# Kernel optimization log

Hardware: AMD Instinct MI355X
Metric: run time of the kernel (lower is better)

## Reference

```python
import jax, jax.numpy as jnp
import numpy as np

N_CLASS = 4432          # 1108 siRNA classes x 4 cell types
N_GROUPS = 4
GROUP_SIZE = N_CLASS // N_GROUPS  # 1108
LABEL_SMOOTHING = 0.1
CONFIDENCE = 1.0 - LABEL_SMOOTHING
SMOOTHING_VALUE = LABEL_SMOOTHING / (GROUP_SIZE - 1)


def setup_inputs() -> dict:
    key = jax.random.key(0)
    k1, k2 = jax.random.split(key)
    output = jax.random.normal(k1, (16384, N_CLASS), dtype=jnp.float32)
    target = jax.random.randint(k2, (16384,), 0, N_CLASS, dtype=jnp.int64)
    return {"output": output, "target": target}


def reference(output, target):
    # output: [B, C] logits, target: [B] int labels
    log_output = jax.nn.log_softmax(output, axis=1)                      # [B, C]
    classes = jnp.arange(N_CLASS, dtype=target.dtype)                    # [C]
    one_hot = jnp.where(classes[None, :] == target[:, None],
                        CONFIDENCE, SMOOTHING_VALUE).astype(output.dtype)  # [B, C]
    # group of each class (4 cell-type groups, contiguous blocks of GROUP_SIZE)
    class_group = classes // GROUP_SIZE                                  # [C]
    target_group = target // GROUP_SIZE                                  # [B]
    # zero smoothed mass for classes outside the sample's group (masks[group])
    one_hot = jnp.where(class_group[None, :] == target_group[:, None], one_hot, 0.0)
    loss = -(one_hot * log_output).sum(axis=1)                           # [B]
    return jnp.mean(loss)
```

## Files before the change

kernel.cpp:

```cpp
#include <hip/hip_runtime.h>
#include <math.h>

#define N_CLASS   4432
#define GROUP_SZ  1108
#define NV4       (N_CLASS / 4)
#define GV4       (GROUP_SZ / 4)
#define NROWS     16384
#define BLOCK     256
#define FULL_IT   17
#define TAIL_BASE (FULL_IT * 64)
#define TAIL_N    (NV4 - TAIL_BASE)

static constexpr float CONF   = 0.9f;
static constexpr float SMOOTH = 0.1f / (GROUP_SZ - 1);

typedef float v4f __attribute__((ext_vector_type(4)));

template <bool WS_MODE>
__global__ __launch_bounds__(BLOCK)
void lsl_kernel(const float* __restrict__ logits,
                const int*   __restrict__ target,
                float*       __restrict__ sink) {
    const int wave = threadIdx.x >> 6;
    const int lane = threadIdx.x & 63;
    const int row  = (NROWS - 1) - (blockIdx.x * 4 + wave);
    const v4f* __restrict__ rp = (const v4f*)(logits + (size_t)row * N_CLASS);

    const int t      = target[row];
    const int g      = t / GROUP_SZ;
    const int glo    = g * GV4;
    const int ghi    = glo + GV4;
    const int tchunk = t >> 2;
    const int tlane  = t & 3;

    v4f v[FULL_IT + 1];
    #pragma unroll
    for (int i = 0; i < FULL_IT; ++i)
        v[i] = __builtin_nontemporal_load(&rp[lane + 64 * i]);
    const bool have18 = (lane < TAIL_N);
    v[FULL_IT] = (v4f){-INFINITY, -INFINITY, -INFINITY, -INFINITY};
    if (have18) v[FULL_IT] = __builtin_nontemporal_load(&rp[TAIL_BASE + lane]);

    float m = -INFINITY;
    #pragma unroll
    for (int i = 0; i <= FULL_IT; ++i)
        m = fmaxf(m, fmaxf(fmaxf(v[i].x, v[i].y), fmaxf(v[i].z, v[i].w)));
    #pragma unroll
    for (int off = 32; off > 0; off >>= 1)
        m = fmaxf(m, __shfl_xor(m, off));

    float s = 0.f;
    #pragma unroll
    for (int i = 0; i <= FULL_IT; ++i) {
        s += __expf(v[i].x - m) + __expf(v[i].y - m)
           + __expf(v[i].z - m) + __expf(v[i].w - m);
    }

    float gsum = 0.f, xt = 0.f;
    #pragma unroll
    for (int i = 0; i <= FULL_IT; ++i) {
        const int  c     = (i < FULL_IT) ? (lane + 64 * i) : (TAIL_BASE + lane);
        const bool valid = (i < FULL_IT) || have18;
        if (valid && c >= glo && c < ghi)
            gsum += (v[i].x + v[i].y) + (v[i].z + v[i].w);
        if (valid && c == tchunk)
            xt = (tlane == 0) ? v[i].x : (tlane == 1) ? v[i].y
               : (tlane == 2) ? v[i].z : v[i].w;
    }

    #pragma unroll
    for (int off = 32; off > 0; off >>= 1) {
        s    += __shfl_xor(s, off);
        gsum += __shfl_xor(gsum, off);
        xt   += __shfl_xor(xt, off);
    }

    if (lane == 0) {
        const float loss = (m + __logf(s)) - ((CONF - SMOOTH) * xt + SMOOTH * gsum);
        if (WS_MODE) sink[row] = loss;
        else         atomicAdd(sink, loss * (1.0f / NROWS));
    }
}

__global__ __launch_bounds__(256)
void lsl_reduce(const float* __restrict__ ws, float* __restrict__ out) {
    const float4* wp = (const float4*)ws;
    const int tid = threadIdx.x;
    float s = 0.f;
    #pragma unroll
    for (int i = 0; i < NROWS / 4 / 256; ++i) {
        float4 v = wp[tid + i * 256];
        s += (v.x + v.y) + (v.z + v.w);
    }
    #pragma unroll
    for (int off = 32; off > 0; off >>= 1) s += __shfl_xor(s, off);
    __shared__ float ss[4];
    const int wave = tid >> 6, lane = tid & 63;
    if (lane == 0) ss[wave] = s;
    __syncthreads();
    if (tid == 0) out[0] = ((ss[0] + ss[1]) + (ss[2] + ss[3])) * (1.0f / NROWS);
}

extern "C" void kernel_launch(void* const* d_in, const int* in_sizes, int n_in,
                              void* d_out, int out_size, void* d_ws, size_t ws_size,
                              hipStream_t stream) {
    const float* logits = (const float*)d_in[0];
    const int*   target = (const int*)d_in[1];
    float*       result = (float*)d_out;
    float*       ws     = (float*)d_ws;

    if (ws_size >= (size_t)NROWS * sizeof(float)) {
        lsl_kernel<true><<<NROWS / 4, BLOCK, 0, stream>>>(logits, target, ws);
        lsl_reduce<<<1, 256, 0, stream>>>(ws, result);
    } else {
        hipMemsetAsync(result, 0, sizeof(float), stream);
        lsl_kernel<false><<<NROWS / 4, BLOCK, 0, stream>>>(logits, target, result);
    }
}
```

Measured before the change: 356.0 us.

## Map one row per 256-thread block with shared-memory cross-wave reduction

Measured after the change: 382.1 us. 1.07x slower.

```diff
diff --git a/kernel.cpp b/kernel.cpp
--- a/kernel.cpp
+++ b/kernel.cpp
@@ -7,9 +7,8 @@
 #define GV4       (GROUP_SZ / 4)
 #define NROWS     16384
 #define BLOCK     256
-#define FULL_IT   17
-#define TAIL_BASE (FULL_IT * 64)
-#define TAIL_N    (NV4 - TAIL_BASE)
+#define CPT       4
+#define TAIL_T    (NV4 - CPT * BLOCK)
 
 static constexpr float CONF   = 0.9f;
 static constexpr float SMOOTH = 0.1f / (GROUP_SZ - 1);
@@ -17,14 +16,20 @@
 typedef float v4f __attribute__((ext_vector_type(4)));
 
 template <bool WS_MODE>
-__global__ __launch_bounds__(BLOCK)
+__global__ __launch_bounds__(BLOCK, 8)
 void lsl_kernel(const float* __restrict__ logits,
                 const int*   __restrict__ target,
                 float*       __restrict__ sink) {
-    const int wave = threadIdx.x >> 6;
-    const int lane = threadIdx.x & 63;
-    const int row  = (NROWS - 1) - (blockIdx.x * 4 + wave);
+    const int tid = threadIdx.x;
+    const int row = (NROWS - 1) - blockIdx.x;
     const v4f* __restrict__ rp = (const v4f*)(logits + (size_t)row * N_CLASS);
+
+    v4f v[CPT + 1];
+    #pragma unroll
+    for (int i = 0; i < CPT; ++i) v[i] = rp[tid + BLOCK * i];
+    const bool have5 = (tid < TAIL_T);
+    v[CPT] = (v4f){-INFINITY, -INFINITY, -INFINITY, -INFINITY};
+    if (have5) v[CPT] = rp[tid + BLOCK * CPT];
 
     const int t      = target[row];
     const int g      = t / GROUP_SZ;
@@ -33,49 +38,46 @@
     const int tchunk = t >> 2;
     const int tlane  = t & 3;
 
-    v4f v[FULL_IT + 1];
-    #pragma unroll
-    for (int i = 0; i < FULL_IT; ++i)
-        v[i] = __builtin_nontemporal_load(&rp[lane + 64 * i]);
-    const bool have18 = (lane < TAIL_N);
-    v[FULL_IT] = (v4f){-INFINITY, -INFINITY, -INFINITY, -INFINITY};
-    if (have18) v[FULL_IT] = __builtin_nontemporal_load(&rp[TAIL_BASE + lane]);
-
     float m = -INFINITY;
     #pragma unroll
-    for (int i = 0; i <= FULL_IT; ++i)
+    for (int i = 0; i <= CPT; ++i)
         m = fmaxf(m, fmaxf(fmaxf(v[i].x, v[i].y), fmaxf(v[i].z, v[i].w)));
     #pragma unroll
     for (int off = 32; off > 0; off >>= 1)
         m = fmaxf(m, __shfl_xor(m, off));
 
-    float s = 0.f;
+    __shared__ float sm[4];
+    __shared__ float sr[4][3];
+    const int wave = tid >> 6, lane = tid & 63;
+    if (lane == 0) sm[wave] = m;
+    __syncthreads();
+    m = fmaxf(fmaxf(sm[0], sm[1]), fmaxf(sm[2], sm[3]));
+
+    float s = 0.f, gsum = 0.f, xt = 0.f;
     #pragma unroll
-    for (int i = 0; i <= FULL_IT; ++i) {
+    for (int i = 0; i <= CPT; ++i) {
         s += __expf(v[i].x - m) + __expf(v[i].y - m)
            + __expf(v[i].z - m) + __expf(v[i].w - m);
-    }
-
-    float gsum = 0.f, xt = 0.f;
-    #pragma unroll
-    for (int i = 0; i <= FULL_IT; ++i) {
-        const int  c     = (i < FULL_IT) ? (lane + 64 * i) : (TAIL_BASE + lane);
-        const bool valid = (i < FULL_IT) || have18;
+        const int  c     = tid + BLOCK * i;
+        const bool valid = (i < CPT) || have5;
         if (valid && c >= glo && c < ghi)
             gsum += (v[i].x + v[i].y) + (v[i].z + v[i].w);
         if (valid && c == tchunk)
             xt = (tlane == 0) ? v[i].x : (tlane == 1) ? v[i].y
                : (tlane == 2) ? v[i].z : v[i].w;
     }
-
     #pragma unroll
     for (int off = 32; off > 0; off >>= 1) {
         s    += __shfl_xor(s, off);
         gsum += __shfl_xor(gsum, off);
         xt   += __shfl_xor(xt, off);
     }
-
-    if (lane == 0) {
+    if (lane == 0) { sr[wave][0] = s; sr[wave][1] = gsum; sr[wave][2] = xt; }
+    __syncthreads();
+    if (tid == 0) {
+        s    = (sr[0][0] + sr[1][0]) + (sr[2][0] + sr[3][0]);
+        gsum = (sr[0][1] + sr[1][1]) + (sr[2][1] + sr[3][1]);
+        xt   = (sr[0][2] + sr[1][2]) + (sr[2][2] + sr[3][2]);
         const float loss = (m + __logf(s)) - ((CONF - SMOOTH) * xt + SMOOTH * gsum);
         if (WS_MODE) sink[row] = loss;
         else         atomicAdd(sink, loss * (1.0f / NROWS));
@@ -110,10 +112,10 @@
     float*       ws     = (float*)d_ws;
 
     if (ws_size >= (size_t)NROWS * sizeof(float)) {
-        lsl_kernel<true><<<NROWS / 4, BLOCK, 0, stream>>>(logits, target, ws);
+        lsl_kernel<true><<<NROWS, BLOCK, 0, stream>>>(logits, target, ws);
         lsl_reduce<<<1, 256, 0, stream>>>(ws, result);
     } else {
         hipMemsetAsync(result, 0, sizeof(float), stream);
-        lsl_kernel<false><<<NROWS / 4, BLOCK, 0, stream>>>(logits, target, result);
+        lsl_kernel<false><<<NROWS, BLOCK, 0, stream>>>(logits, target, result);
     }
 }
```
